# Kernel optimization log

Measured on AMD Instinct MI355X. Metric: run time of the kernel, lower is better.

## Reference

```python
import jax, jax.numpy as jnp
import numpy as np

BATCH_SIZE = 8192   # args.batch_size
NUM_VIEWS = 2       # args.num_views
TEMPERATURE = 0.07  # args.loss_args['temperature']
FEAT_DIM = 256
N = (BATCH_SIZE // 2) * NUM_VIEWS  # rows of features


def _static_index_maps():
    # labels = sorted cat of num_views copies of arange(batch_size//2)
    labels = np.sort(np.tile(np.arange(BATCH_SIZE // 2), NUM_VIEWS))
    lab_mat = labels[None, :] == labels[:, None]          # (N, N) bool
    # off-diagonal column indices: for row i, columns [0..N-1] excluding i,
    # in ascending order (matches torch boolean-mask extraction order)
    j = np.arange(N - 1)
    cols = j[None, :] + (j[None, :] >= np.arange(N)[:, None])  # (N, N-1)
    lab_off = np.take_along_axis(lab_mat, cols, axis=1)        # (N, N-1) bool
    k = NUM_VIEWS - 1  # positives per row
    # stable sort puts positive positions first, preserving column order
    order = np.argsort(~lab_off, axis=1, kind='stable')
    pos_cols = order[:, :k]   # (N, k)
    neg_cols = order[:, k:]   # (N, N-1-k)
    return cols, pos_cols, neg_cols

_COLS, _POS_COLS, _NEG_COLS = _static_index_maps()


def setup_inputs() -> dict:
    key = jax.random.key(0)
    features = jax.random.normal(key, (N, FEAT_DIM), dtype=jnp.float32)
    return {"features": features}


def reference(features):
    # L2 normalize rows (F.normalize eps clamp)
    norm = jnp.maximum(jnp.linalg.norm(features, axis=1, keepdims=True), 1e-12)
    f = features / norm
    sim = f @ f.T                                            # (N, N)
    sim_off = jnp.take_along_axis(sim, jnp.asarray(_COLS), axis=1)       # (N, N-1)
    positives = jnp.take_along_axis(sim_off, jnp.asarray(_POS_COLS), axis=1)
    negatives = jnp.take_along_axis(sim_off, jnp.asarray(_NEG_COLS), axis=1)
    logits = jnp.concatenate([positives, negatives], axis=1) / TEMPERATURE
    # CrossEntropyLoss with target class 0 for every row
    loss = jnp.mean(-jax.nn.log_softmax(logits, axis=1)[:, 0])
    return loss
```

## Files before the change

kernel.cpp:

```cpp
#include <hip/hip_runtime.h>
#include <stdint.h>

#define N_ROWS 8192
#define FEAT   256
#define YSPLIT 16
#define CPB    (N_ROWS / YSPLIT)
#define CT     64
#define LDS_STRIDE 264

typedef __bf16 bf16x8 __attribute__((ext_vector_type(8)));
typedef float  f32x4  __attribute__((ext_vector_type(4)));

__device__ __forceinline__ unsigned short f2bf(float x) {
    union { float f; uint32_t u; } v; v.f = x;
    uint32_t u = v.u;
    return (unsigned short)((u + 0x7FFFu + ((u >> 16) & 1u)) >> 16);
}

__global__ void knorm(const float* __restrict__ feat,
                      unsigned short* __restrict__ fb,
                      float* __restrict__ pos) {
    __shared__ float ex[4][FEAT];
    int wave = threadIdx.x >> 6;
    int lane = threadIdx.x & 63;
    int row  = blockIdx.x * 4 + wave;
    float4 v = ((const float4*)(feat + row * FEAT))[lane];
    float ss = v.x*v.x + v.y*v.y + v.z*v.z + v.w*v.w;
    #pragma unroll
    for (int off = 1; off < 64; off <<= 1) ss += __shfl_xor(ss, off);
    float inv = 1.0f / fmaxf(sqrtf(ss), 1e-12f);
    float4 o; o.x = v.x*inv; o.y = v.y*inv; o.z = v.z*inv; o.w = v.w*inv;
    ushort4 b;
    b.x = f2bf(o.x); b.y = f2bf(o.y); b.z = f2bf(o.z); b.w = f2bf(o.w);
    ((ushort4*)(fb + row * FEAT))[lane] = b;
    ((float4*)ex[wave])[lane] = o;
    __syncthreads();
    float4 p = ((float4*)ex[wave ^ 1])[lane];
    float d = o.x*p.x + o.y*p.y + o.z*p.z + o.w*p.w;
    #pragma unroll
    for (int off = 1; off < 64; off <<= 1) d += __shfl_xor(d, off);
    if (lane == 0) pos[row] = d;
}

__global__ __launch_bounds__(512)
void kmain(const unsigned short* __restrict__ fb, float* __restrict__ partial) {
    __shared__ unsigned short Bs[CT][LDS_STRIDE];
    const int t    = threadIdx.x;
    const int lane = t & 63;
    const int wave = t >> 6;
    const int quad = lane >> 4;
    const int l15  = lane & 15;
    const int rw    = blockIdx.x * 256 + wave * 32;
    const int cbase = blockIdx.y * CPB;
    const float Kc = 20.60992915555662f;

    bf16x8 af[2][8];
    #pragma unroll
    for (int rf = 0; rf < 2; ++rf)
        #pragma unroll
        for (int ks = 0; ks < 8; ++ks) {
            int row = rw + rf * 16 + l15;
            int k   = ks * 32 + quad * 8;
            af[rf][ks] = *(const bf16x8*)(fb + row * FEAT + k);
        }

    float lsum[2][4] = {{0.f,0.f,0.f,0.f},{0.f,0.f,0.f,0.f}};

    for (int ct = 0; ct < CPB / CT; ++ct) {
        __syncthreads();
        const int c0 = cbase + ct * CT;
        #pragma unroll
        for (int i = 0; i < 4; ++i) {
            int idx = t + i * 512;
            int r = idx >> 5;
            int o = (idx & 31) * 8;
            *(uint4*)(&Bs[r][o]) = *(const uint4*)(fb + (c0 + r) * FEAT + o);
        }
        __syncthreads();

        #pragma unroll
        for (int g = 0; g < 4; ++g) {
            const int cg = c0 + g * 16;
            f32x4 acc0 = {0.f,0.f,0.f,0.f};
            f32x4 acc1 = {0.f,0.f,0.f,0.f};
            #pragma unroll
            for (int ks = 0; ks < 8; ++ks) {
                bf16x8 b = *(const bf16x8*)(&Bs[g * 16 + l15][ks * 32 + quad * 8]);
                acc0 = __builtin_amdgcn_mfma_f32_16x16x32_bf16(af[0][ks], b, acc0, 0, 0, 0);
                acc1 = __builtin_amdgcn_mfma_f32_16x16x32_bf16(af[1][ks], b, acc1, 0, 0, 0);
            }
            const bool dg = (cg < rw + 32) && (cg + 16 > rw);
            const int C = cg + l15;
            #pragma unroll
            for (int r = 0; r < 4; ++r) {
                float e0 = __builtin_amdgcn_exp2f(fmaf(acc0[r], Kc, -Kc));
                float e1 = __builtin_amdgcn_exp2f(fmaf(acc1[r], Kc, -Kc));
                if (dg) {
                    int R0 = rw + quad * 4 + r;
                    if (R0 == C)      e0 = 0.f;
                    if (R0 + 16 == C) e1 = 0.f;
                }
                lsum[0][r] += e0;
                lsum[1][r] += e1;
            }
        }
    }

    #pragma unroll
    for (int rf = 0; rf < 2; ++rf)
        #pragma unroll
        for (int r = 0; r < 4; ++r) {
            float v = lsum[rf][r];
            v += __shfl_xor(v, 1);
            v += __shfl_xor(v, 2);
            v += __shfl_xor(v, 4);
            v += __shfl_xor(v, 8);
            lsum[rf][r] = v;
        }
    if (l15 == 0) {
        #pragma unroll
        for (int rf = 0; rf < 2; ++rf)
            #pragma unroll
            for (int r = 0; r < 4; ++r) {
                int row = rw + rf * 16 + quad * 4 + r;
                partial[blockIdx.y * N_ROWS + row] = lsum[rf][r];
            }
    }
}

__global__ void kreduce(const float* __restrict__ partial,
                        const float* __restrict__ pos,
                        float* __restrict__ bsum) {
    __shared__ float red[4];
    int row  = blockIdx.x * 256 + threadIdx.x;
    int wave = threadIdx.x >> 6;
    int lane = threadIdx.x & 63;
    float L = 0.f;
    #pragma unroll
    for (int p = 0; p < YSPLIT; ++p) L += partial[p * N_ROWS + row];
    const float invT = 14.285714285714286f;
    float loss = invT * (1.0f - pos[row])
               + 0.6931471805599453f * __builtin_amdgcn_logf(L);
    #pragma unroll
    for (int off = 1; off < 64; off <<= 1) loss += __shfl_xor(loss, off);
    if (lane == 0) red[wave] = loss;
    __syncthreads();
    if (threadIdx.x == 0)
        bsum[blockIdx.x] = red[0] + red[1] + red[2] + red[3];
}

__global__ void kfinal(const float* __restrict__ bsum, float* __restrict__ out) {
    int lane = threadIdx.x;
    float v = (lane < 32) ? bsum[lane] : 0.f;
    #pragma unroll
    for (int off = 1; off < 32; off <<= 1) v += __shfl_xor(v, off);
    if (lane == 0) out[0] = v * (1.0f / 8192.0f);
}

extern "C" void kernel_launch(void* const* d_in, const int* in_sizes, int n_in,
                              void* d_out, int out_size, void* d_ws, size_t ws_size,
                              hipStream_t stream) {
    const float* feat = (const float*)d_in[0];
    float* out = (float*)d_out;
    char* ws = (char*)d_ws;
    unsigned short* fb      = (unsigned short*)ws;
    float*          partial = (float*)(ws + (4u << 20));
    float*          pos     = (float*)(ws + (4u << 20) + (1u << 19));
    float*          bsum    = (float*)(ws + (4u << 20) + (1u << 19) + (1u << 15));

    knorm<<<N_ROWS / 4, 256, 0, stream>>>(feat, fb, pos);
    kmain<<<dim3(32, YSPLIT), 512, 0, stream>>>(fb, partial);
    kreduce<<<N_ROWS / 256, 256, 0, stream>>>(partial, pos, bsum);
    kfinal<<<1, 64, 0, stream>>>(bsum, out);
}
```

Baseline: 104.5 us.

## Switch similarity GEMM to FP8 MFMA with larger per-wave row tiles

Normalized features are now quantized to FP8 (scaled by 16) instead of bf16, and the main kernel uses the fp8 16x16x32 MFMA, with the scale folded into the exp2 constant. Each wave now covers 64 rows instead of 32, so every B fragment loaded from LDS feeds four MFMAs, and the column split is doubled to keep the grid size. This halves memory and LDS traffic and raises MFMA throughput, at the cost of lower precision in the similarity logits, which are multiplied by about 20 before exponentiation. The diagonal masking check is simplified to match the new 16-row tiles.

```diff
diff --git a/kernel.cpp b/kernel.cpp
--- a/kernel.cpp
+++ b/kernel.cpp
@@ -3,22 +3,15 @@
 
 #define N_ROWS 8192
 #define FEAT   256
-#define YSPLIT 16
+#define YSPLIT 32
 #define CPB    (N_ROWS / YSPLIT)
 #define CT     64
-#define LDS_STRIDE 264
+#define BSTRIDE 280
 
-typedef __bf16 bf16x8 __attribute__((ext_vector_type(8)));
-typedef float  f32x4  __attribute__((ext_vector_type(4)));
-
-__device__ __forceinline__ unsigned short f2bf(float x) {
-    union { float f; uint32_t u; } v; v.f = x;
-    uint32_t u = v.u;
-    return (unsigned short)((u + 0x7FFFu + ((u >> 16) & 1u)) >> 16);
-}
+typedef float f32x4 __attribute__((ext_vector_type(4)));
 
 __global__ void knorm(const float* __restrict__ feat,
-                      unsigned short* __restrict__ fb,
+                      uint32_t* __restrict__ f8,
                       float* __restrict__ pos) {
     __shared__ float ex[4][FEAT];
     int wave = threadIdx.x >> 6;
@@ -30,101 +23,96 @@
     for (int off = 1; off < 64; off <<= 1) ss += __shfl_xor(ss, off);
     float inv = 1.0f / fmaxf(sqrtf(ss), 1e-12f);
     float4 o; o.x = v.x*inv; o.y = v.y*inv; o.z = v.z*inv; o.w = v.w*inv;
-    ushort4 b;
-    b.x = f2bf(o.x); b.y = f2bf(o.y); b.z = f2bf(o.z); b.w = f2bf(o.w);
-    ((ushort4*)(fb + row * FEAT))[lane] = b;
+    const float s = 16.0f;
+    uint32_t p = __builtin_amdgcn_cvt_pk_fp8_f32(o.x*s, o.y*s, 0, false);
+    p = __builtin_amdgcn_cvt_pk_fp8_f32(o.z*s, o.w*s, p, true);
+    f8[row * (FEAT/4) + lane] = p;
     ((float4*)ex[wave])[lane] = o;
     __syncthreads();
-    float4 p = ((float4*)ex[wave ^ 1])[lane];
-    float d = o.x*p.x + o.y*p.y + o.z*p.z + o.w*p.w;
+    float4 q = ((float4*)ex[wave ^ 1])[lane];
+    float d = o.x*q.x + o.y*q.y + o.z*q.z + o.w*q.w;
     #pragma unroll
     for (int off = 1; off < 64; off <<= 1) d += __shfl_xor(d, off);
     if (lane == 0) pos[row] = d;
 }
 
-__global__ __launch_bounds__(512)
-void kmain(const unsigned short* __restrict__ fb, float* __restrict__ partial) {
-    __shared__ unsigned short Bs[CT][LDS_STRIDE];
+__global__ __launch_bounds__(512, 4)
+void kmain(const uint8_t* __restrict__ f8, float* __restrict__ partial) {
+    __shared__ uint8_t Bs[CT * BSTRIDE];
     const int t    = threadIdx.x;
     const int lane = t & 63;
     const int wave = t >> 6;
     const int quad = lane >> 4;
     const int l15  = lane & 15;
-    const int rw    = blockIdx.x * 256 + wave * 32;
+    const int rw    = blockIdx.x * 512 + wave * 64;
     const int cbase = blockIdx.y * CPB;
     const float Kc = 20.60992915555662f;
+    const float Ks = Kc / 256.0f;
 
-    bf16x8 af[2][8];
+    long af[4][8];
     #pragma unroll
-    for (int rf = 0; rf < 2; ++rf)
+    for (int rg = 0; rg < 4; ++rg)
         #pragma unroll
-        for (int ks = 0; ks < 8; ++ks) {
-            int row = rw + rf * 16 + l15;
-            int k   = ks * 32 + quad * 8;
-            af[rf][ks] = *(const bf16x8*)(fb + row * FEAT + k);
-        }
+        for (int ks = 0; ks < 8; ++ks)
+            af[rg][ks] = *(const long*)(f8 + (rw + rg*16 + l15) * FEAT + ks*32 + quad*8);
 
-    float lsum[2][4] = {{0.f,0.f,0.f,0.f},{0.f,0.f,0.f,0.f}};
+    float lsum[4][4] = {};
 
     for (int ct = 0; ct < CPB / CT; ++ct) {
         __syncthreads();
         const int c0 = cbase + ct * CT;
-        #pragma unroll
-        for (int i = 0; i < 4; ++i) {
-            int idx = t + i * 512;
-            int r = idx >> 5;
-            int o = (idx & 31) * 8;
-            *(uint4*)(&Bs[r][o]) = *(const uint4*)(fb + (c0 + r) * FEAT + o);
+        {
+            int col = t >> 3;
+            int o   = (t & 7) * 32;
+            const ulonglong2* src = (const ulonglong2*)(f8 + (c0 + col) * FEAT + o);
+            ulonglong2 w0 = src[0];
+            ulonglong2 w1 = src[1];
+            uint64_t* dst = (uint64_t*)(Bs + col * BSTRIDE + o);
+            dst[0] = w0.x; dst[1] = w0.y; dst[2] = w1.x; dst[3] = w1.y;
         }
         __syncthreads();
 
         #pragma unroll
         for (int g = 0; g < 4; ++g) {
-            const int cg = c0 + g * 16;
-            f32x4 acc0 = {0.f,0.f,0.f,0.f};
-            f32x4 acc1 = {0.f,0.f,0.f,0.f};
+            f32x4 acc[4] = {{0,0,0,0},{0,0,0,0},{0,0,0,0},{0,0,0,0}};
             #pragma unroll
             for (int ks = 0; ks < 8; ++ks) {
-                bf16x8 b = *(const bf16x8*)(&Bs[g * 16 + l15][ks * 32 + quad * 8]);
-                acc0 = __builtin_amdgcn_mfma_f32_16x16x32_bf16(af[0][ks], b, acc0, 0, 0, 0);
-                acc1 = __builtin_amdgcn_mfma_f32_16x16x32_bf16(af[1][ks], b, acc1, 0, 0, 0);
+                long b = *(const long*)(Bs + (g*16 + l15) * BSTRIDE + ks*32 + quad*8);
+                #pragma unroll
+                for (int rg = 0; rg < 4; ++rg)
+                    acc[rg] = __builtin_amdgcn_mfma_f32_16x16x32_fp8_fp8(af[rg][ks], b, acc[rg], 0, 0, 0);
             }
-            const bool dg = (cg < rw + 32) && (cg + 16 > rw);
-            const int C = cg + l15;
+            const int cg = c0 + g * 16;
             #pragma unroll
-            for (int r = 0; r < 4; ++r) {
-                float e0 = __builtin_amdgcn_exp2f(fmaf(acc0[r], Kc, -Kc));
-                float e1 = __builtin_amdgcn_exp2f(fmaf(acc1[r], Kc, -Kc));
-                if (dg) {
-                    int R0 = rw + quad * 4 + r;
-                    if (R0 == C)      e0 = 0.f;
-                    if (R0 + 16 == C) e1 = 0.f;
+            for (int rg = 0; rg < 4; ++rg) {
+                const bool dg = (cg == rw + rg * 16);
+                #pragma unroll
+                for (int r = 0; r < 4; ++r) {
+                    float e = __builtin_amdgcn_exp2f(fmaf(acc[rg][r], Ks, -Kc));
+                    if (dg && l15 == quad * 4 + r) e = 0.f;
+                    lsum[rg][r] += e;
                 }
-                lsum[0][r] += e0;
-                lsum[1][r] += e1;
             }
         }
     }
 
     #pragma unroll
-    for (int rf = 0; rf < 2; ++rf)
+    for (int rg = 0; rg < 4; ++rg)
         #pragma unroll
         for (int r = 0; r < 4; ++r) {
-            float v = lsum[rf][r];
+            float v = lsum[rg][r];
             v += __shfl_xor(v, 1);
             v += __shfl_xor(v, 2);
             v += __shfl_xor(v, 4);
             v += __shfl_xor(v, 8);
-            lsum[rf][r] = v;
+            lsum[rg][r] = v;
         }
     if (l15 == 0) {
         #pragma unroll
-        for (int rf = 0; rf < 2; ++rf)
+        for (int rg = 0; rg < 4; ++rg)
             #pragma unroll
-            for (int r = 0; r < 4; ++r) {
-                int row = rw + rf * 16 + quad * 4 + r;
-                partial[blockIdx.y * N_ROWS + row] = lsum[rf][r];
-            }
+            for (int r = 0; r < 4; ++r)
+                partial[blockIdx.y * N_ROWS + rw + rg*16 + quad*4 + r] = lsum[rg][r];
     }
 }
 
@@ -163,13 +151,13 @@
     const float* feat = (const float*)d_in[0];
     float* out = (float*)d_out;
     char* ws = (char*)d_ws;
-    unsigned short* fb      = (unsigned short*)ws;
-    float*          partial = (float*)(ws + (4u << 20));
-    float*          pos     = (float*)(ws + (4u << 20) + (1u << 19));
-    float*          bsum    = (float*)(ws + (4u << 20) + (1u << 19) + (1u << 15));
+    uint32_t* f8      = (uint32_t*)ws;
+    float*    partial = (float*)(ws + (2u << 20));
+    float*    pos     = (float*)(ws + (3u << 20));
+    float*    bsum    = (float*)(ws + (3u << 20) + (1u << 15));
 
-    knorm<<<N_ROWS / 4, 256, 0, stream>>>(feat, fb, pos);
-    kmain<<<dim3(32, YSPLIT), 512, 0, stream>>>(fb, partial);
+    knorm<<<N_ROWS / 4, 256, 0, stream>>>(feat, f8, pos);
+    kmain<<<dim3(16, YSPLIT), 512, 0, stream>>>((const uint8_t*)f8, partial);
     kreduce<<<N_ROWS / 256, 256, 0, stream>>>(partial, pos, bsum);
     kfinal<<<1, 64, 0, stream>>>(bsum, out);
 }
```

Result: slower. 143.3 us (+37.2%).
